# Kernel optimization log

Hardware: AMD Instinct MI355X
Metric: run time of the kernel (lower is better)

## Reference

```python
import math
import jax, jax.numpy as jnp
import numpy as np

N = 4096        # num nodes
IN_DIM = 512
H0 = 64         # hidden_dim[0]
H1 = 64         # hidden_dim[-1]
HEADS = 4
N_CLASSES = 10


def setup_inputs() -> dict:
    key = jax.random.key(0)
    ks = jax.random.split(key, 10)
    feats = jax.random.normal(ks[0], (N, IN_DIM), dtype=jnp.float32)
    counting_attn = jax.random.uniform(ks[1], (N, N), dtype=jnp.float32)
    s1 = 1.0 / math.sqrt(IN_DIM)
    s2 = 1.0 / math.sqrt(H0 * HEADS)
    # layer-1 heads, stacked: [H, out, in] (torch Linear weight layout)
    Wq1 = jax.random.normal(ks[2], (HEADS, H0, IN_DIM), dtype=jnp.float32) * s1
    Wk1 = jax.random.normal(ks[3], (HEADS, H0, IN_DIM), dtype=jnp.float32) * s1
    Wv1 = jax.random.normal(ks[4], (HEADS, H0, IN_DIM), dtype=jnp.float32) * s1
    # layer-2 single head: [out, in]
    Wq2 = jax.random.normal(ks[5], (H1, H0 * HEADS), dtype=jnp.float32) * s2
    Wk2 = jax.random.normal(ks[6], (H1, H0 * HEADS), dtype=jnp.float32) * s2
    Wv2 = jax.random.normal(ks[7], (H1, H0 * HEADS), dtype=jnp.float32) * s2
    Wc = jax.random.normal(ks[8], (N_CLASSES, H1), dtype=jnp.float32) * (1.0 / math.sqrt(H1))
    bc = jax.random.normal(ks[9], (N_CLASSES,), dtype=jnp.float32) * 0.01
    return {"feats": feats, "counting_attn": counting_attn,
            "Wq1": Wq1, "Wk1": Wk1, "Wv1": Wv1,
            "Wq2": Wq2, "Wk2": Wk2, "Wv2": Wv2,
            "Wc": Wc, "bc": bc}


def _gkat_heads(feat, Wq, Wk, Wv, counting):
    # feat: [N, in], Wq/Wk/Wv: [H, d, in], counting: [N, N] -> [N, H*d]
    Q = jnp.einsum('ni,hdi->hnd', feat, Wq)
    K = jnp.einsum('ni,hdi->hnd', feat, Wk)
    V = jnp.einsum('ni,hdi->hnd', feat, Wv)
    d = Q.shape[-1]
    logits = jnp.einsum('hnd,hmd->hnm', Q, K) / jnp.sqrt(jnp.asarray(d, Q.dtype))
    e = jnp.exp(logits - jnp.max(logits, axis=-1, keepdims=True))
    a = jnp.einsum('hnm,mk->hnk', e, counting)          # exp(logits) @ counting_attn
    a = a / (jnp.sum(a, axis=-1, keepdims=True) + 1e-9)  # row-normalize
    ret = jnp.einsum('hnm,hmd->hnd', a, V)
    ret = jax.nn.elu(ret)
    H, n, dd = ret.shape
    return jnp.transpose(ret, (1, 0, 2)).reshape(n, H * dd)  # concat heads along dim=1


def reference(feats, counting_attn, Wq1, Wk1, Wv1, Wq2, Wk2, Wv2, Wc, bc):
    # normalize over feature dim (torch.std is unbiased -> ddof=1)
    mean_ = jnp.mean(feats, axis=1, keepdims=True)
    std_ = jnp.std(feats, axis=1, keepdims=True, ddof=1)
    h = (feats - mean_) / (std_ + 1e-9)
    h = _gkat_heads(h, Wq1, Wk1, Wv1, counting_attn)                 # [N, H*H0]
    h = _gkat_heads(h, Wq2[None], Wk2[None], Wv2[None], counting_attn)  # [N, H1]
    return h @ Wc.T + bc
```

## Files before the change

kernel.cpp:

```cpp
#include <hip/hip_runtime.h>
#include <hip/hip_bf16.h>
#include <math.h>

#define NN4   4096
#define QSCALE 0.180336880111120420f

typedef __attribute__((ext_vector_type(8))) short short8;
typedef __attribute__((ext_vector_type(8))) unsigned short ushort8;
typedef __attribute__((ext_vector_type(4))) unsigned short ushort4v;
typedef __attribute__((ext_vector_type(4))) float f32x4;

__device__ __forceinline__ unsigned short f2b(float f) {
  union { __hip_bfloat16 h; unsigned short u; } v;
  v.h = __float2bfloat16(f);
  return v.u;
}
__device__ __forceinline__ float b2f(unsigned short s) {
  return __uint_as_float(((unsigned int)s) << 16);
}
__device__ __forceinline__ ushort8 cvt8(f32x4 a, f32x4 b) {
  return (ushort8){f2b(a[0]), f2b(a[1]), f2b(a[2]), f2b(a[3]),
                   f2b(b[0]), f2b(b[1]), f2b(b[2]), f2b(b[3])};
}

#define GLOAD16(gp, lp) __builtin_amdgcn_global_load_lds( \
    (const __attribute__((address_space(1))) void*)(gp),  \
    (__attribute__((address_space(3))) void*)(lp), 16, 0, 0)

__global__ __launch_bounds__(256) void k_norm(const float* __restrict__ x,
                                              unsigned short* __restrict__ y) {
  int row  = blockIdx.x * 4 + (threadIdx.x >> 6);
  int lane = threadIdx.x & 63;
  const float4* src = (const float4*)(x + (size_t)row * 512);
  float4 a = src[lane];
  float4 b = src[lane + 64];
  float s = a.x + a.y + a.z + a.w + b.x + b.y + b.z + b.w;
#pragma unroll
  for (int off = 32; off; off >>= 1) s += __shfl_xor(s, off);
  float mean = s * (1.0f / 512.0f);
  float ssq = 0.f, d;
  d = a.x - mean; ssq += d * d;  d = a.y - mean; ssq += d * d;
  d = a.z - mean; ssq += d * d;  d = a.w - mean; ssq += d * d;
  d = b.x - mean; ssq += d * d;  d = b.y - mean; ssq += d * d;
  d = b.z - mean; ssq += d * d;  d = b.w - mean; ssq += d * d;
#pragma unroll
  for (int off = 32; off; off >>= 1) ssq += __shfl_xor(ssq, off);
  float inv = 1.0f / (sqrtf(ssq * (1.0f / 511.0f)) + 1e-9f);
  unsigned short* dst = y + (size_t)row * 512;
  ushort4v va = (ushort4v){f2b((a.x - mean) * inv), f2b((a.y - mean) * inv),
                           f2b((a.z - mean) * inv), f2b((a.w - mean) * inv)};
  ushort4v vb = (ushort4v){f2b((b.x - mean) * inv), f2b((b.y - mean) * inv),
                           f2b((b.z - mean) * inv), f2b((b.w - mean) * inv)};
  *(ushort4v*)(dst + lane * 4)       = va;
  *(ushort4v*)(dst + 256 + lane * 4) = vb;
}

__global__ __launch_bounds__(256) void k_cvtcnt(const float* __restrict__ in,
                                                unsigned short* __restrict__ out) {
  size_t i = ((size_t)blockIdx.x * 256 + threadIdx.x) * 8;
  const size_t stride = (size_t)gridDim.x * 256 * 8;
  for (; i < (size_t)4096 * 4096; i += stride) {
    f32x4 a = *(const f32x4*)(in + i);
    f32x4 b = *(const f32x4*)(in + i + 4);
    *(ushort8*)(out + i) = cvt8(a, b);
  }
}

__global__ __launch_bounds__(256) void k_projqkv(
    const unsigned short* __restrict__ Ap, int K,
    const float* __restrict__ Wq, const float* __restrict__ Wk,
    const float* __restrict__ Wv, int N, int nT,
    unsigned short* __restrict__ Qo, unsigned short* __restrict__ Ko,
    unsigned short* __restrict__ VT, int padrows, float qscale) {
  __shared__ unsigned short As[128 * 40];
  __shared__ unsigned short Bs[128 * 40];
  const int tid = threadIdx.x;
  const int sel = blockIdx.y / nT;
  const int n0 = (blockIdx.y % nT) * 128;
  const int m0 = blockIdx.x * 128;
  const float* Bp = sel == 0 ? Wq : (sel == 1 ? Wk : Wv);
  const float bscale = sel == 0 ? qscale : 1.0f;
  const int lane = tid & 63, wid = tid >> 6;
  const int hi = lane >> 4, lo = lane & 15;
  const int wr = (wid >> 1) << 6, wc = (wid & 1) << 6;
  const int srow = tid >> 1, sk = (tid & 1) << 4;
  f32x4 acc[4][4];
#pragma unroll
  for (int i = 0; i < 4; ++i)
#pragma unroll
    for (int j = 0; j < 4; ++j) acc[i][j] = (f32x4){0.f, 0.f, 0.f, 0.f};

  for (int k0 = 0; k0 < K; k0 += 32) {
    ushort8 va0, va1, vb0, vb1;
    {
      const unsigned short* s = Ap + (size_t)(m0 + srow) * K + k0 + sk;
      va0 = *(const ushort8*)(s);
      va1 = *(const ushort8*)(s + 8);
    }
    {
      int gr = n0 + srow;
      if (gr < N) {
        const float* s = Bp + (size_t)gr * K + k0 + sk;
        f32x4 f0 = *(const f32x4*)(s) * bscale;
        f32x4 f1 = *(const f32x4*)(s + 4) * bscale;
        f32x4 f2 = *(const f32x4*)(s + 8) * bscale;
        f32x4 f3 = *(const f32x4*)(s + 12) * bscale;
        vb0 = cvt8(f0, f1); vb1 = cvt8(f2, f3);
      } else { vb0 = (ushort8)0; vb1 = (ushort8)0; }
    }
    __syncthreads();
    *(ushort8*)&As[srow * 40 + sk]     = va0;
    *(ushort8*)&As[srow * 40 + sk + 8] = va1;
    *(ushort8*)&Bs[srow * 40 + sk]     = vb0;
    *(ushort8*)&Bs[srow * 40 + sk + 8] = vb1;
    __syncthreads();
    short8 af[4], bf[4];
#pragma unroll
    for (int i = 0; i < 4; ++i)
      af[i] = *(const short8*)&As[(wr + (i << 4) + lo) * 40 + hi * 8];
#pragma unroll
    for (int j = 0; j < 4; ++j)
      bf[j] = *(const short8*)&Bs[(wc + (j << 4) + lo) * 40 + hi * 8];
#pragma unroll
    for (int i = 0; i < 4; ++i)
#pragma unroll
      for (int j = 0; j < 4; ++j)
        acc[i][j] = __builtin_amdgcn_mfma_f32_16x16x32_bf16(af[i], bf[j], acc[i][j], 0, 0, 0);
  }

  if (sel < 2) {
    unsigned short* Cp = sel == 0 ? Qo : Ko;
#pragma unroll
    for (int i = 0; i < 4; ++i)
#pragma unroll
      for (int j = 0; j < 4; ++j)
#pragma unroll
        for (int reg = 0; reg < 4; ++reg) {
          int r = m0 + wr + (i << 4) + (hi << 2) + reg;
          int c = n0 + wc + (j << 4) + lo;
          if (c < N) Cp[(size_t)r * N + c] = f2b(acc[i][j][reg]);
        }
  } else {
#pragma unroll
    for (int i = 0; i < 4; ++i)
#pragma unroll
      for (int j = 0; j < 4; ++j) {
        int c = n0 + wc + (j << 4) + lo;
        if (c < N) {
          int hh = c >> 6, dd = c & 63;
          int rb = m0 + wr + (i << 4) + (hi << 2);
          ushort4v pk = (ushort4v){f2b(acc[i][j][0]), f2b(acc[i][j][1]),
                                   f2b(acc[i][j][2]), f2b(acc[i][j][3])};
          *(ushort4v*)&VT[(size_t)(hh * 68 + dd) * NN4 + rb] = pk;
        }
      }
    int hstart = n0 >> 6;
    int hcnt = (N - n0) >> 6; if (hcnt > 2) hcnt = 2;
    int tot = hcnt * padrows * 128;
    for (int e = tid; e < tot; e += 256) {
      int hh = hstart + e / (padrows * 128);
      int rem = e % (padrows * 128);
      int j = rem >> 7, col = m0 + (rem & 127);
      VT[(size_t)(hh * 68 + 64 + j) * NN4 + col] = (j == 0) ? 0x3F80 : 0;
    }
  }
}

template<int NF, int MINW>
__global__ __launch_bounds__(256, MINW) void k_cvxg(
    const unsigned short* __restrict__ cntB,
    const unsigned short* __restrict__ Bt,
    unsigned short* __restrict__ Pb) {
  constexpr int LDB = NF * 16;
  __shared__ unsigned short As[2][4096];
  __shared__ unsigned short Bs[2][NF * 512];
  const int tid = threadIdx.x, lane = tid & 63, wid = tid >> 6;
  const int hi = lane >> 4, lo = lane & 15;
  const int m0 = blockIdx.x * 128;
  const int kbeg = blockIdx.y << 8, kend = kbeg + 256;
  const int boff = (lo * 64 + hi * 16) ^ (((lo >> 1) & 3) << 4);

  f32x4 acc[2][NF];
#pragma unroll
  for (int i = 0; i < 2; ++i)
#pragma unroll
    for (int j = 0; j < NF; ++j) acc[i][j] = (f32x4){0.f, 0.f, 0.f, 0.f};

  auto STAGE = [&](int k0, int buf) {
#pragma unroll
    for (int s = 0; s < 2; ++s) {
      int ch = s * 4 + wid;
      int row = ch * 16 + (lane >> 2);
      int hia = (lane & 3) ^ ((row >> 1) & 3);
      GLOAD16(cntB + (size_t)(m0 + row) * 4096 + k0 + hia * 8,
              (char*)&As[buf][0] + ch * 1024);
    }
    for (int c = wid; c < NF; c += 4) {
      int P = c * 1024 + lane * 16;
      int L = P ^ ((P >> 3) & 0x30);
      GLOAD16(Bt + (size_t)(L >> 6) * 4096 + k0 + ((L & 63) >> 1),
              (char*)&Bs[buf][0] + c * 1024);
    }
  };

  STAGE(kbeg, 0);
  asm volatile("s_waitcnt vmcnt(0)" ::: "memory");
  __syncthreads();

  const int r0 = 32 * wid + lo, r1 = r0 + 16;
  const int ho = ((hi ^ ((r0 >> 1) & 3)) << 3);

  for (int k0 = kbeg; k0 < kend; k0 += 32) {
    const int cur = ((k0 - kbeg) >> 5) & 1, nxt = cur ^ 1;
    if (k0 + 32 < kend) STAGE(k0 + 32, nxt);
    short8 af0 = *(const short8*)&As[cur][r0 * 32 + ho];
    short8 af1 = *(const short8*)&As[cur][r1 * 32 + ho];
    __builtin_amdgcn_s_setprio(1);
#pragma unroll
    for (int j = 0; j < NF; ++j) {
      short8 bf = *(const short8*)((const char*)&Bs[cur][0] + j * 1024 + boff);
      acc[0][j] = __builtin_amdgcn_mfma_f32_16x16x32_bf16(af0, bf, acc[0][j], 0, 0, 0);
      acc[1][j] = __builtin_amdgcn_mfma_f32_16x16x32_bf16(af1, bf, acc[1][j], 0, 0, 0);
    }
    __builtin_amdgcn_s_setprio(0);
    asm volatile("s_waitcnt vmcnt(0)" ::: "memory");
    __syncthreads();
  }
  unsigned short* P = Pb + (size_t)blockIdx.y * 4096 * LDB;
#pragma unroll
  for (int i = 0; i < 2; ++i)
#pragma unroll
    for (int j = 0; j < NF; ++j)
#pragma unroll
      for (int reg = 0; reg < 4; ++reg) {
        int r = m0 + 32 * wid + 16 * i + 4 * hi + reg;
        P[(size_t)r * LDB + 16 * j + lo] = f2b(acc[i][j][reg]);
      }
}

__global__ __launch_bounds__(256) void k_tredB(const unsigned short* __restrict__ in, int ld,
                                               int nsl, unsigned short* __restrict__ out,
                                               int orow) {
  __shared__ float t[64][65];
  const int n0 = blockIdx.x << 6, d0 = blockIdx.y << 6;
  const int o  = threadIdx.x & 7;
  const int rr = threadIdx.x >> 3;
  const size_t pstride = (size_t)4096 * ld;
  const bool valid = (o * 8) < (ld - d0);
#pragma unroll
  for (int pass = 0; pass < 2; ++pass) {
    const int r = rr + (pass << 5);
    float a[8] = {0.f, 0.f, 0.f, 0.f, 0.f, 0.f, 0.f, 0.f};
    if (valid) {
      const unsigned short* p = in + (size_t)(n0 + r) * ld + d0 + o * 8;
      for (int z = 0; z < nsl; ++z) {
        ushort8 v = *(const ushort8*)(p + (size_t)z * pstride);
#pragma unroll
        for (int k = 0; k < 8; ++k) a[k] += b2f(v[k]);
      }
    }
#pragma unroll
    for (int k = 0; k < 8; ++k) t[o * 8 + k][r] = a[k];
  }
  __syncthreads();
  const int c = threadIdx.x & 63, r4 = threadIdx.x >> 6;
#pragma unroll
  for (int i = 0; i < 16; ++i) {
    int dr = r4 + (i << 2);
    if (d0 + dr < orow)
      out[(size_t)(d0 + dr) * 4096 + n0 + c] = f2b(t[dr][c]);
  }
}

__global__ __launch_bounds__(256, 2) void k_attn(
    const unsigned short* __restrict__ Qg, const unsigned short* __restrict__ Kg,
    int ldqk, const unsigned short* __restrict__ CVg,
    unsigned short* __restrict__ Pb) {
  __shared__ unsigned short Ks[128 * 72];
  __shared__ unsigned short Cs[80 * 136];
  __shared__ unsigned short Es[128 * 136];
  const int tid = threadIdx.x, lane = tid & 63, wid = tid >> 6;
  const int hi = lane >> 4, lo = lane & 15;
  const int qb = blockIdx.x, h = blockIdx.y, sl = blockIdx.z;
  const int n0 = qb * 128;
  const int MS = 4096 / gridDim.z;
  const int m0beg = sl * MS;
  const int wr = (wid >> 1) << 6, wc = (wid & 1) << 6;

  short8 qf[4][2];
  const unsigned short* Qh = Qg + (size_t)h * 64;
#pragma unroll
  for (int j = 0; j < 4; ++j)
#pragma unroll
    for (int t = 0; t < 2; ++t)
      qf[j][t] = *(const short8*)(Qh + (size_t)(n0 + wc + 16 * j + lo) * ldqk + t * 32 + hi * 8);

  const unsigned short* CVh = CVg + (size_t)h * 68 * NN4;
  const unsigned short* Kh  = Kg + (size_t)h * 64;

  const int krow = tid >> 1, khalf = (tid & 1) << 5;
  int crdR[5], crdW[5], ccol[5];
#pragma unroll
  for (int k = 0; k < 5; ++k) {
    int c = tid + k * 256;
    int row = c >> 4;
    crdW[k] = row;
    crdR[k] = row < 68 ? row : 67;
    ccol[k] = (c & 15) << 3;
  }
  ushort8 krg[4], crg[5];

  auto LOADK = [&](int m0) {
    const unsigned short* src = Kh + (size_t)(m0 + krow) * ldqk + khalf;
    krg[0] = *(const ushort8*)(src);
    krg[1] = *(const ushort8*)(src + 8);
    krg[2] = *(const ushort8*)(src + 16);
    krg[3] = *(const ushort8*)(src + 24);
  };
  auto LOADC = [&](int m0) {
#pragma unroll
    for (int k = 0; k < 5; ++k)
      crg[k] = *(const ushort8*)(CVh + (size_t)crdR[k] * NN4 + m0 + ccol[k]);
  };
  auto WRITEK = [&]() {
    unsigned short* dp = &Ks[krow * 72 + khalf];
    *(ushort8*)(dp) = krg[0];      *(ushort8*)(dp + 8) = krg[1];
    *(ushort8*)(dp + 16) = krg[2]; *(ushort8*)(dp + 24) = krg[3];
  };
  auto WRITEC = [&]() {
#pragma unroll
    for (int k = 0; k < 5; ++k)
      *(ushort8*)&Cs[crdW[k] * 136 + ccol[k]] = crg[k];
  };

  f32x4 accn[2][5];
#pragma unroll
  for (int i = 0; i < 2; ++i)
#pragma unroll
    for (int j = 0; j < 5; ++j) accn[i][j] = (f32x4){0.f, 0.f, 0.f, 0.f};

  LOADK(m0beg); LOADC(m0beg);
  WRITEK(); WRITEC();
  __syncthreads();

  for (int mt = 0; mt < MS; mt += 128) {
    const int m0 = m0beg + mt;
    const bool more = (mt + 128) < MS;
    if (more) { LOADK(m0 + 128); LOADC(m0 + 128); }
    short8 kf[4][2];
#pragma unroll
    for (int i = 0; i < 4; ++i)
#pragma unroll
      for (int t = 0; t < 2; ++t)
        kf[i][t] = *(const short8*)&Ks[(wr + 16 * i + lo) * 72 + t * 32 + hi * 8];
    f32x4 s[4][4];
#pragma unroll
    for (int i = 0; i < 4; ++i)
#pragma unroll
      for (int j = 0; j < 4; ++j) s[i][j] = (f32x4){0.f, 0.f, 0.f, 0.f};
    __builtin_amdgcn_s_setprio(1);
#pragma unroll
    for (int t = 0; t < 2; ++t)
#pragma unroll
      for (int i = 0; i < 4; ++i)
#pragma unroll
        for (int j = 0; j < 4; ++j)
          s[i][j] = __builtin_amdgcn_mfma_f32_16x16x32_bf16(kf[i][t], qf[j][t], s[i][j], 0, 0, 0);
    __builtin_amdgcn_s_setprio(0);
#pragma unroll
    for (int i = 0; i < 4; ++i)
#pragma unroll
      for (int j = 0; j < 4; ++j) {
        unsigned int u0 = (unsigned int)f2b(__builtin_amdgcn_exp2f(s[i][j][0])) |
                          ((unsigned int)f2b(__builtin_amdgcn_exp2f(s[i][j][1])) << 16);
        unsigned int u1 = (unsigned int)f2b(__builtin_amdgcn_exp2f(s[i][j][2])) |
                          ((unsigned int)f2b(__builtin_amdgcn_exp2f(s[i][j][3])) << 16);
        unsigned long long pk = (unsigned long long)u0 | ((unsigned long long)u1 << 32);
        int row = wc + 16 * j + lo;
        int byte = row * 272 + (wr + 16 * i + 4 * hi) * 2;
        *(unsigned long long*)((char*)Es + (byte ^ ((row & 7) << 5))) = pk;
      }
    __syncthreads();
    if (more) WRITEK();
    __builtin_amdgcn_s_setprio(1);
#pragma unroll
    for (int t2 = 0; t2 < 4; ++t2) {
      int r0 = 32 * wid + lo, r1 = r0 + 16;
      int cb = (t2 * 32 + hi * 8) * 2;
      short8 ea0 = *(const short8*)((const char*)Es + ((r0 * 272 + cb) ^ ((r0 & 7) << 5)));
      short8 ea1 = *(const short8*)((const char*)Es + ((r1 * 272 + cb) ^ ((r1 & 7) << 5)));
      short8 cbv[5];
#pragma unroll
      for (int j2 = 0; j2 < 5; ++j2)
        cbv[j2] = *(const short8*)&Cs[(16 * j2 + lo) * 136 + t2 * 32 + hi * 8];
#pragma unroll
      for (int j2 = 0; j2 < 5; ++j2) {
        accn[0][j2] = __builtin_amdgcn_mfma_f32_16x16x32_bf16(ea0, cbv[j2], accn[0][j2], 0, 0, 0);
        accn[1][j2] = __builtin_amdgcn_mfma_f32_16x16x32_bf16(ea1, cbv[j2], accn[1][j2], 0, 0, 0);
      }
    }
    __builtin_amdgcn_s_setprio(0);
    __syncthreads();
    if (more) { WRITEC(); __syncthreads(); }
  }
  unsigned short* P = Pb + (((size_t)h * gridDim.x + qb) * gridDim.z + sl) * (128 * 80);
#pragma unroll
  for (int i2 = 0; i2 < 2; ++i2)
#pragma unroll
    for (int j2 = 0; j2 < 5; ++j2)
#pragma unroll
      for (int reg = 0; reg < 4; ++reg) {
        int r = 32 * wid + 16 * i2 + 4 * hi + reg;
        int c = 16 * j2 + lo;
        P[(size_t)r * 80 + c] = f2b(accn[i2][j2][reg]);
      }
}

__global__ void k_fin2(const unsigned short* __restrict__ parts, int nsl,
                       unsigned short* __restrict__ hb, int ldh) {
  int idx = blockIdx.x * 256 + threadIdx.x;
  int d = idx & 63, r = (idx >> 6) & 4095, h = idx >> 18;
  size_t b0 = ((size_t)(h * 32 + (r >> 7)) * nsl) * 10240 + (size_t)(r & 127) * 80;
  float nm = 0.f, dn = 0.f;
  for (int sl = 0; sl < nsl; ++sl) {
    const unsigned short* p = parts + b0 + (size_t)sl * 10240;
    nm += b2f(p[d]); dn += b2f(p[64]);
  }
  float x = nm / (dn + 1e-9f);
  x = x > 0.f ? x : expm1f(x);
  hb[(size_t)r * ldh + h * 64 + d] = f2b(x);
}

__global__ __launch_bounds__(256) void k_fincls(const unsigned short* __restrict__ parts,
                                                int nsl, const float* __restrict__ Wc,
                                                const float* __restrict__ bc,
                                                float* __restrict__ out) {
  int r = blockIdx.x * 4 + (threadIdx.x >> 6);
  int d = threadIdx.x & 63;
  size_t b0 = ((size_t)(r >> 7) * nsl) * 10240 + (size_t)(r & 127) * 80;
  float nm = 0.f, dn = 0.f;
  for (int sl = 0; sl < nsl; ++sl) {
    const unsigned short* p = parts + b0 + (size_t)sl * 10240;
    nm += b2f(p[d]); dn += b2f(p[64]);
  }
  float x = nm / (dn + 1e-9f);
  x = x > 0.f ? x : expm1f(x);
#pragma unroll
  for (int cl = 0; cl < 10; ++cl) {
    float v = x * Wc[cl * 64 + d];
#pragma unroll
    for (int off = 32; off; off >>= 1) v += __shfl_xor(v, off);
    if (d == 0) out[(size_t)r * 10 + cl] = v + bc[cl];
  }
}

extern "C" void kernel_launch(void* const* d_in, const int* in_sizes, int n_in,
                              void* d_out, int out_size, void* d_ws, size_t ws_size,
                              hipStream_t stream) {
  (void)in_sizes; (void)n_in; (void)out_size; (void)ws_size;
  const float* feats    = (const float*)d_in[0];
  const float* counting = (const float*)d_in[1];
  const float* Wq1 = (const float*)d_in[2];
  const float* Wk1 = (const float*)d_in[3];
  const float* Wv1 = (const float*)d_in[4];
  const float* Wq2 = (const float*)d_in[5];
  const float* Wk2 = (const float*)d_in[6];
  const float* Wv2 = (const float*)d_in[7];
  const float* Wc  = (const float*)d_in[8];
  const float* bc  = (const float*)d_in[9];
  float* out = (float*)d_out;

  char* w = (char*)d_ws;
  size_t off = 0;
  auto alloc = [&](size_t bytes) { void* p = w + off; off += (bytes + 255) & ~(size_t)255; return p; };
  unsigned short* hnb    = (unsigned short*)alloc((size_t)4096 * 512 * 2);
  unsigned short* Q1b    = (unsigned short*)alloc((size_t)4096 * 256 * 2);
  unsigned short* K1b    = (unsigned short*)alloc((size_t)4096 * 256 * 2);
  unsigned short* V1xT   = (unsigned short*)alloc((size_t)272 * 4096 * 2);
  unsigned short* CVX1Tb = (unsigned short*)alloc((size_t)272 * 4096 * 2);
  unsigned short* h1b    = (unsigned short*)alloc((size_t)4096 * 256 * 2);
  unsigned short* Q2b    = (unsigned short*)alloc((size_t)4096 * 64 * 2);
  unsigned short* K2b    = (unsigned short*)alloc((size_t)4096 * 64 * 2);
  unsigned short* V2xT   = (unsigned short*)alloc((size_t)80 * 4096 * 2);
  unsigned short* CVX2Tb = (unsigned short*)alloc((size_t)68 * 4096 * 2);
  unsigned short* cntB   = (unsigned short*)alloc((size_t)4096 * 4096 * 2);
  unsigned short* big    = (unsigned short*)alloc((size_t)36 * 1024 * 1024);

  k_norm<<<1024, 256, 0, stream>>>(feats, hnb);
  k_cvtcnt<<<2048, 256, 0, stream>>>(counting, cntB);

  k_projqkv<<<dim3(32, 6), 256, 0, stream>>>(hnb, 512, Wq1, Wk1, Wv1, 256, 2,
                                             Q1b, K1b, V1xT, 4, QSCALE);
  k_cvxg<17, 3><<<dim3(32, 16), 256, 0, stream>>>(cntB, V1xT, big);
  k_tredB<<<dim3(64, 5), 256, 0, stream>>>(big, 272, 16, CVX1Tb, 272);
  k_attn<<<dim3(32, 4, 4), 256, 0, stream>>>(Q1b, K1b, 256, CVX1Tb, big);
  k_fin2<<<4096, 256, 0, stream>>>(big, 4, h1b, 256);

  k_projqkv<<<dim3(32, 3), 256, 0, stream>>>(h1b, 256, Wq2, Wk2, Wv2, 64, 1,
                                             Q2b, K2b, V2xT, 16, QSCALE);
  k_cvxg<5, 4><<<dim3(32, 16), 256, 0, stream>>>(cntB, V2xT, big);
  k_tredB<<<dim3(64, 2), 256, 0, stream>>>(big, 80, 16, CVX2Tb, 68);
  k_attn<<<dim3(32, 1, 16), 256, 0, stream>>>(Q2b, K2b, 64, CVX2Tb, big);
  k_fincls<<<1024, 256, 0, stream>>>(big, 16, Wc, bc, out);
}
```

Before: 175.1 us.

## Triple-buffer cvxg GEMM pipeline with counted vmcnt waits and single barrier

```diff
diff --git a/kernel.cpp b/kernel.cpp
--- a/kernel.cpp
+++ b/kernel.cpp
@@ -172,12 +172,12 @@
     const unsigned short* __restrict__ Bt,
     unsigned short* __restrict__ Pb) {
   constexpr int LDB = NF * 16;
-  __shared__ unsigned short As[2][4096];
-  __shared__ unsigned short Bs[2][NF * 512];
+  __shared__ unsigned short As[3][4096];
+  __shared__ unsigned short Bs[3][NF * 512];
   const int tid = threadIdx.x, lane = tid & 63, wid = tid >> 6;
   const int hi = lane >> 4, lo = lane & 15;
   const int m0 = blockIdx.x * 128;
-  const int kbeg = blockIdx.y << 8, kend = kbeg + 256;
+  const int kbeg = blockIdx.y << 8;
   const int boff = (lo * 64 + hi * 16) ^ (((lo >> 1) & 3) << 4);
 
   f32x4 acc[2][NF];
@@ -186,7 +186,8 @@
 #pragma unroll
     for (int j = 0; j < NF; ++j) acc[i][j] = (f32x4){0.f, 0.f, 0.f, 0.f};
 
-  auto STAGE = [&](int k0, int buf) {
+  auto STAGE = [&](int t, int buf) {
+    const int k0 = kbeg + t * 32;
 #pragma unroll
     for (int s = 0; s < 2; ++s) {
       int ch = s * 4 + wid;
@@ -203,29 +204,43 @@
     }
   };
 
-  STAGE(kbeg, 0);
-  asm volatile("s_waitcnt vmcnt(0)" ::: "memory");
-  __syncthreads();
-
   const int r0 = 32 * wid + lo, r1 = r0 + 16;
   const int ho = ((hi ^ ((r0 >> 1) & 3)) << 3);
 
-  for (int k0 = kbeg; k0 < kend; k0 += 32) {
-    const int cur = ((k0 - kbeg) >> 5) & 1, nxt = cur ^ 1;
-    if (k0 + 32 < kend) STAGE(k0 + 32, nxt);
-    short8 af0 = *(const short8*)&As[cur][r0 * 32 + ho];
-    short8 af1 = *(const short8*)&As[cur][r1 * 32 + ho];
+  auto COMPUTE = [&](int buf) {
+    short8 af0 = *(const short8*)&As[buf][r0 * 32 + ho];
+    short8 af1 = *(const short8*)&As[buf][r1 * 32 + ho];
     __builtin_amdgcn_s_setprio(1);
 #pragma unroll
     for (int j = 0; j < NF; ++j) {
-      short8 bf = *(const short8*)((const char*)&Bs[cur][0] + j * 1024 + boff);
+      short8 bf = *(const short8*)((const char*)&Bs[buf][0] + j * 1024 + boff);
       acc[0][j] = __builtin_amdgcn_mfma_f32_16x16x32_bf16(af0, bf, acc[0][j], 0, 0, 0);
       acc[1][j] = __builtin_amdgcn_mfma_f32_16x16x32_bf16(af1, bf, acc[1][j], 0, 0, 0);
     }
     __builtin_amdgcn_s_setprio(0);
-    asm volatile("s_waitcnt vmcnt(0)" ::: "memory");
-    __syncthreads();
-  }
+  };
+
+  const bool extra = wid < (NF & 3);
+
+  STAGE(0, 0);
+  STAGE(1, 1);
+
+  for (int t = 0; t < 7; ++t) {
+    if constexpr (NF == 17) {
+      if (extra) asm volatile("s_waitcnt vmcnt(7)" ::: "memory");
+      else       asm volatile("s_waitcnt vmcnt(6)" ::: "memory");
+    } else {
+      if (extra) asm volatile("s_waitcnt vmcnt(4)" ::: "memory");
+      else       asm volatile("s_waitcnt vmcnt(3)" ::: "memory");
+    }
+    __builtin_amdgcn_s_barrier();
+    if (t + 2 < 8) STAGE(t + 2, (t + 2) % 3);
+    COMPUTE(t % 3);
+  }
+  asm volatile("s_waitcnt vmcnt(0)" ::: "memory");
+  __builtin_amdgcn_s_barrier();
+  COMPUTE(7 % 3);
+
   unsigned short* P = Pb + (size_t)blockIdx.y * 4096 * LDB;
 #pragma unroll
   for (int i = 0; i < 2; ++i)
@@ -491,7 +506,7 @@
 
   k_projqkv<<<dim3(32, 6), 256, 0, stream>>>(hnb, 512, Wq1, Wk1, Wv1, 256, 2,
                                              Q1b, K1b, V1xT, 4, QSCALE);
-  k_cvxg<17, 3><<<dim3(32, 16), 256, 0, stream>>>(cntB, V1xT, big);
+  k_cvxg<17, 2><<<dim3(32, 16), 256, 0, stream>>>(cntB, V1xT, big);
   k_tredB<<<dim3(64, 5), 256, 0, stream>>>(big, 272, 16, CVX1Tb, 272);
   k_attn<<<dim3(32, 4, 4), 256, 0, stream>>>(Q1b, K1b, 256, CVX1Tb, big);
   k_fin2<<<4096, 256, 0, stream>>>(big, 4, h1b, 256);
```

Result: no change. 173.8 us (-0.7%).
